# Kernel optimization log

Measured on AMD Instinct MI355X. Metric: run time of the kernel, lower is better.

## Reference

```python
import jax, jax.numpy as jnp
import numpy as np

N_TILES, NX = 6, 96
IN_C, HID_C = 128, 256
BATCH = 4


def _build_neighbors(n_tiles=N_TILES, nx=NX):
    # 4-connectivity on each tile with periodic wrap (fixed cubed-sphere-style
    # grid graph; preserves the gather/mean access pattern of build_dgl_graph).
    i, j = np.meshgrid(np.arange(nx), np.arange(nx), indexing='ij')
    idx = lambda ii, jj: (ii % nx) * nx + (jj % nx)
    per_tile = np.stack([idx(i - 1, j), idx(i + 1, j), idx(i, j - 1), idx(i, j + 1)],
                        axis=-1).reshape(nx * nx, 4)
    offsets = (np.arange(n_tiles) * nx * nx)[:, None, None]
    return (per_tile[None] + offsets).reshape(-1, 4).astype(np.int32)


def setup_inputs() -> dict:
    key = jax.random.key(0)
    ks = jax.random.split(key, 6)
    s = lambda fan_in: 1.0 / np.sqrt(fan_in)
    return {
        'x': jax.random.normal(ks[0], (BATCH, N_TILES, NX, NX, IN_C), jnp.float32),
        'neighbors': jnp.asarray(_build_neighbors()),
        'W_self1': jax.random.normal(ks[1], (IN_C, HID_C), jnp.float32) * s(IN_C),
        'W_neigh1': jax.random.normal(ks[2], (IN_C, HID_C), jnp.float32) * s(IN_C),
        'b1': jnp.zeros((HID_C,), jnp.float32),
        'W_self2': jax.random.normal(ks[3], (HID_C, HID_C), jnp.float32) * s(HID_C),
        'W_neigh2': jax.random.normal(ks[4], (HID_C, HID_C), jnp.float32) * s(HID_C),
        'b2': jnp.zeros((HID_C,), jnp.float32),
    }


def _sage_conv(h, neighbors, W_self, W_neigh, b):
    # h: [B, N, C]; neighbors: [N, 4] -> mean-aggregated SAGEConv
    h_neigh = jnp.mean(h[:, neighbors], axis=2)  # [B, N, 4, C] -> [B, N, C]
    return jnp.einsum('bnc,cd->bnd', h, W_self) + \
           jnp.einsum('bnc,cd->bnd', h_neigh, W_neigh) + b


def reference(x, neighbors, W_self1, W_neigh1, b1, W_self2, W_neigh2, b2):
    B, T, X, Y, C = x.shape
    h = x.reshape(B, T * X * Y, C)                      # flatten sphere -> nodes
    h = jax.nn.relu(_sage_conv(h, neighbors, W_self1, W_neigh1, b1))
    h = jax.nn.relu(_sage_conv(h, neighbors, W_self2, W_neigh2, b2))
    return h.reshape(B, T, X, Y, -1)
```

## Files before the change

kernel.cpp:

```cpp
#include <hip/hip_runtime.h>
#include <stdint.h>

typedef __attribute__((ext_vector_type(8))) short short8;
typedef __attribute__((ext_vector_type(4))) float f32x4;

#define NNODES 55296
#define DOUT 256

#define WAIT_VM(N) asm volatile("s_waitcnt vmcnt(" #N ")" ::: "memory")
#define SOFT_FENCE asm volatile("" ::: "memory")

__device__ __forceinline__ float bf2f(unsigned short h) {
    union { unsigned u; float f; } x; x.u = ((unsigned)h) << 16; return x.f;
}
__device__ __forceinline__ unsigned short f2bf(float f) {
    union { float f; unsigned u; } x; x.f = f;
    return (unsigned short)((x.u + 0x7fffu + ((x.u >> 16) & 1u)) >> 16);
}

__device__ __forceinline__ void storev(float* p, float v) { *p = v; }
__device__ __forceinline__ void storev(unsigned short* p, float v) { *p = f2bf(v); }

__device__ __forceinline__ void dma16(const void* g, void* l) {
    __builtin_amdgcn_global_load_lds(
        reinterpret_cast<const unsigned int __attribute__((address_space(1)))*>((uintptr_t)g),
        reinterpret_cast<unsigned int __attribute__((address_space(3)))*>((uintptr_t)l),
        16, 0, 0);
}

__device__ __forceinline__ short8 frag_self(const float* p) {
    float4 a = *(const float4*)p, b = *(const float4*)(p + 4);
    union { short8 s; unsigned short u[8]; } r;
    r.u[0] = f2bf(a.x); r.u[1] = f2bf(a.y); r.u[2] = f2bf(a.z); r.u[3] = f2bf(a.w);
    r.u[4] = f2bf(b.x); r.u[5] = f2bf(b.y); r.u[6] = f2bf(b.z); r.u[7] = f2bf(b.w);
    return r.s;
}
__device__ __forceinline__ short8 frag_self(const unsigned short* p) {
    return *(const short8*)p;
}
__device__ __forceinline__ void acc8(const float* p, float* o) {
    float4 a = *(const float4*)p, b = *(const float4*)(p + 4);
    o[0] += a.x; o[1] += a.y; o[2] += a.z; o[3] += a.w;
    o[4] += b.x; o[5] += b.y; o[6] += b.z; o[7] += b.w;
}
__device__ __forceinline__ void acc8(const unsigned short* p, float* o) {
    uint4 v = *(const uint4*)p;
    const unsigned short* u = (const unsigned short*)&v;
#pragma unroll
    for (int i = 0; i < 8; ++i) o[i] += bf2f(u[i]);
}
template <typename TIN>
__device__ __forceinline__ short8 frag_mean4(const TIN* p0, const TIN* p1,
                                             const TIN* p2, const TIN* p3) {
    float s[8] = {0.f, 0.f, 0.f, 0.f, 0.f, 0.f, 0.f, 0.f};
    acc8(p0, s); acc8(p1, s); acc8(p2, s); acc8(p3, s);
    union { short8 s8; unsigned short u[8]; } r;
#pragma unroll
    for (int i = 0; i < 8; ++i) r.u[i] = f2bf(s[i] * 0.25f);
    return r.s8;
}

__global__ void build_wt(const float* __restrict__ Ws,
                         const float* __restrict__ Wn,
                         unsigned short* __restrict__ Wt, int C) {
    int K2 = 2 * C;
    int idx = blockIdx.x * 256 + threadIdx.x;
    if (idx >= 256 * K2) return;
    int d = idx / K2;
    int k = idx - d * K2;
    float v = (k < C) ? Ws[(size_t)k * DOUT + d] : Wn[(size_t)(k - C) * DOUT + d];
    Wt[idx] = f2bf(v);
}

__global__ void build_wt_pm(const float* __restrict__ Ws,
                            const float* __restrict__ Wn,
                            unsigned short* __restrict__ Wp, int C) {
    int K2 = 2 * C;
    int idx = blockIdx.x * 256 + threadIdx.x;
    if (idx >= 256 * K2) return;
    int d = idx / K2;
    int k = idx - d * K2;
    float v = (k < C) ? Ws[(size_t)k * DOUT + d] : Wn[(size_t)(k - C) * DOUT + d];
    int q = k >> 6;
    int kqb = (k & 63) * 2;
    int byte = q * 32768 + d * 128 + (kqb ^ ((d & 7) << 4));
    Wp[byte >> 1] = f2bf(v);
}

__global__ __launch_bounds__(256) void mean_xb_pm(const float* __restrict__ x,
                                                  const int* __restrict__ nbr,
                                                  unsigned short* __restrict__ xm,
                                                  int mTot) {
    const int idx = blockIdx.x * 256 + threadIdx.x;
    const int node = idx >> 4;
    const int ch = (idx & 15) * 8;
    const int b = node / NNODES;
    const int n = node - b * NNODES;
    const size_t bbase = (size_t)b * NNODES;
    const int4 nb = *(const int4*)(nbr + (size_t)n * 4);
    const float* ps = x + (size_t)node * 128 + ch;
    union { uint4 v; unsigned short u[8]; } rs, rm;
    float4 a0 = *(const float4*)ps, a1 = *(const float4*)(ps + 4);
    rs.u[0] = f2bf(a0.x); rs.u[1] = f2bf(a0.y); rs.u[2] = f2bf(a0.z); rs.u[3] = f2bf(a0.w);
    rs.u[4] = f2bf(a1.x); rs.u[5] = f2bf(a1.y); rs.u[6] = f2bf(a1.z); rs.u[7] = f2bf(a1.w);
    float s[8] = {0.f, 0.f, 0.f, 0.f, 0.f, 0.f, 0.f, 0.f};
    acc8(x + (bbase + nb.x) * 128 + ch, s);
    acc8(x + (bbase + nb.y) * 128 + ch, s);
    acc8(x + (bbase + nb.z) * 128 + ch, s);
    acc8(x + (bbase + nb.w) * 128 + ch, s);
#pragma unroll
    for (int i = 0; i < 8; ++i) rm.u[i] = f2bf(s[i] * 0.25f);
    const size_t cs = (size_t)mTot * 32;
    *(uint4*)(xm + (size_t)(ch >> 5) * cs + (size_t)node * 32 + (ch & 31)) = rs.v;
    *(uint4*)(xm + (size_t)(4 + (ch >> 5)) * cs + (size_t)node * 32 + (ch & 31)) = rm.v;
}

__global__ __launch_bounds__(256) void mean_pass_pm(const unsigned short* __restrict__ h1,
                                                    const int* __restrict__ nbr,
                                                    unsigned short* __restrict__ hm,
                                                    int mTot) {
    const int idx = blockIdx.x * 256 + threadIdx.x;
    const int node = idx >> 5;
    const int ch = (idx & 31) * 8;
    const int b = node / NNODES;
    const int n = node - b * NNODES;
    const size_t bbase = (size_t)b * NNODES;
    const int4 nb = *(const int4*)(nbr + (size_t)n * 4);
    const size_t cs = (size_t)mTot * 32;
    const size_t co = (size_t)(ch >> 5) * cs + (ch & 31);
    float s[8] = {0.f, 0.f, 0.f, 0.f, 0.f, 0.f, 0.f, 0.f};
    acc8(h1 + co + (bbase + nb.x) * 32, s);
    acc8(h1 + co + (bbase + nb.y) * 32, s);
    acc8(h1 + co + (bbase + nb.z) * 32, s);
    acc8(h1 + co + (bbase + nb.w) * 32, s);
    union { uint4 v; unsigned short u[8]; } r;
#pragma unroll
    for (int i = 0; i < 8; ++i) r.u[i] = f2bf(s[i] * 0.25f);
    *(uint4*)(hm + co + (size_t)node * 32) = r.v;
}

template <int NK, typename TOUT>
__global__ __launch_bounds__(256) void sage_v15(
    const unsigned short* __restrict__ a0p,
    const unsigned short* __restrict__ a1p,
    const unsigned short* __restrict__ Wp,
    const float* __restrict__ bias,
    TOUT* __restrict__ out,
    int nwg, int mTot) {
    extern __shared__ char lds[];
    const int tid = threadIdx.x;
    const int bid = blockIdx.x;
    const int wk = (bid & 7) * (nwg >> 3) + (bid >> 3);
    const int yg = wk & 1;
    const int rb = wk >> 1;
    const int gcol0 = yg * 128;
    const int rowbase = rb * 128;

    const int l = tid & 63, w = tid >> 6;
    const int lr = l & 15, lg = l >> 4;
    const int rowg = w >> 1;
    const int colb = (w & 1) * 64;

    const size_t chstride = (size_t)mTot * 64;

    auto stageW = [&](int p) {
        char* wb = lds + ((p & 1) << 14);
        const char* src = (const char*)Wp + (size_t)p * 32768 + (size_t)gcol0 * 128;
#pragma unroll
        for (int i = 0; i < 4; ++i) {
            int o = w * 4096 + i * 1024;
            dma16(src + o + l * 16, wb + o + l * 16);
        }
    };
    auto issueA = [&](int p) {
        const char* base = (p >= 4) ? (const char*)a1p : (const char*)a0p;
        const char* src = base + (size_t)((2 * p) & 7) * chstride + (size_t)rowbase * 64;
        char* ring = lds + 32768 + (p % 3) * 16384;
#pragma unroll
        for (int s = 0; s < 2; ++s) {
            const char* cs_ = src + (size_t)s * chstride;
            char* dst = ring + s * 8192;
#pragma unroll
            for (int i = 0; i < 2; ++i) {
                int o = w * 2048 + i * 1024;
                dma16(cs_ + o + l * 16, dst + o + l * 16);
            }
        }
    };

    stageW(0); issueA(0); issueA(1);

    f32x4 acc[4][4];
#pragma unroll
    for (int m = 0; m < 4; ++m)
#pragma unroll
        for (int j = 0; j < 4; ++j) acc[m][j] = (f32x4){0.f, 0.f, 0.f, 0.f};

#pragma unroll
    for (int kk = 0; kk < NK; ++kk) {
        if (kk == NK - 1) { WAIT_VM(0); } else { WAIT_VM(4); }
        __builtin_amdgcn_s_barrier();
        SOFT_FENCE;

        if (kk + 1 < NK) stageW(kk + 1);
        if (kk + 2 < NK) issueA(kk + 2);

        const int ringo = 32768 + (kk % 3) * 16384;
        char* wbuf = lds + ((kk & 1) << 14);
#pragma unroll
        for (int sub = 0; sub < 2; ++sub) {
            short8 af[4];
#pragma unroll
            for (int m = 0; m < 4; ++m)
                af[m] = *(const short8*)(lds + ringo + sub * 8192 +
                                         ((rowg * 4 + m) * 16 + lr) * 64 + lg * 16);
            const int kq0 = (sub << 6) | (lg << 4);
#pragma unroll
            for (int j = 0; j < 4; ++j) {
                const int col = colb + j * 16 + lr;
                const short8 wf = *(const short8*)(
                    wbuf + (col << 7) + (kq0 ^ ((lr & 7) << 4)));
#pragma unroll
                for (int m = 0; m < 4; ++m)
                    acc[m][j] = __builtin_amdgcn_mfma_f32_16x16x32_bf16(wf, af[m], acc[m][j], 0, 0, 0);
            }
        }
        SOFT_FENCE;
    }

#pragma unroll
    for (int m = 0; m < 4; ++m) {
        const int row = rowbase + rowg * 64 + m * 16 + lr;
#pragma unroll
        for (int j = 0; j < 4; ++j) {
            const int gcol = gcol0 + colb + j * 16 + lg * 4;
            const float4 bv = *(const float4*)(bias + gcol);
            float o0 = fmaxf(acc[m][j][0] + bv.x, 0.f);
            float o1 = fmaxf(acc[m][j][1] + bv.y, 0.f);
            float o2 = fmaxf(acc[m][j][2] + bv.z, 0.f);
            float o3 = fmaxf(acc[m][j][3] + bv.w, 0.f);
            if constexpr (sizeof(TOUT) == 4) {
                float4 o = {o0, o1, o2, o3};
                *(float4*)((float*)out + (size_t)row * 256 + gcol) = o;
            } else {
                union { unsigned short u[4]; uint2 v; } pk;
                pk.u[0] = f2bf(o0); pk.u[1] = f2bf(o1);
                pk.u[2] = f2bf(o2); pk.u[3] = f2bf(o3);
                unsigned short* hp = (unsigned short*)out +
                    (size_t)(gcol >> 5) * ((size_t)mTot * 32) +
                    (size_t)row * 32 + (gcol & 31);
                *(uint2*)hp = pk.v;
            }
        }
    }
}

template <int C, typename TIN, typename TOUT>
__global__ __launch_bounds__(512, 2) void sage_v3(
    const TIN* __restrict__ hin, const int* __restrict__ nbr,
    const unsigned short* __restrict__ Wt, const float* __restrict__ bias,
    TOUT* __restrict__ out) {
    constexpr int K2 = 2 * C;
    constexpr int ROWB = K2 * 2;
    constexpr int LCOLS = 131072 / ROWB;
    constexpr int CG = LCOLS / 128;
    constexpr int RG = 8 / CG;
    extern __shared__ char Bs[];

    const int tid = threadIdx.x;
    const int gcol0 = blockIdx.y * LCOLS;
    {
        const char* src = (const char*)(Wt + (size_t)gcol0 * K2);
#pragma unroll
        for (int i = 0; i < 16; ++i) {
            int byt = (i * 512 + tid) * 16;
            uint4 v = *(const uint4*)(src + byt);
            int c = byt / ROWB;
            *(uint4*)(Bs + (byt ^ ((c & 7) << 4))) = v;
        }
    }
    __syncthreads();

    const int l = tid & 63;
    const int w = tid >> 6;
    const int rowg = w / CG;
    const int colb = (w % CG) * 128;
    const int lr = l & 15, lg = l >> 4;

    const int rowbase = blockIdx.x * (RG * 64) + rowg * 64;
    const int bb = rowbase / NNODES;
    const int n0 = rowbase - bb * NNODES;
    const size_t bbase = (size_t)bb * NNODES;

    unsigned soff[4], noff[4][4];
#pragma unroll
    for (int m = 0; m < 4; ++m) {
        int r = m * 16 + lr;
        soff[m] = (unsigned)(((rowbase + r) * (size_t)C + lg * 8) * sizeof(TIN));
        int4 nb = *(const int4*)(nbr + (size_t)(n0 + r) * 4);
        noff[m][0] = (unsigned)(((bbase + nb.x) * C + lg * 8) * sizeof(TIN));
        noff[m][1] = (unsigned)(((bbase + nb.y) * C + lg * 8) * sizeof(TIN));
        noff[m][2] = (unsigned)(((bbase + nb.z) * C + lg * 8) * sizeof(TIN));
        noff[m][3] = (unsigned)(((bbase + nb.w) * C + lg * 8) * sizeof(TIN));
    }
    const char* hb = (const char*)hin;

    f32x4 acc[4][8];
#pragma unroll
    for (int m = 0; m < 4; ++m)
#pragma unroll
        for (int j = 0; j < 8; ++j) acc[m][j] = (f32x4){0.f, 0.f, 0.f, 0.f};

#pragma unroll
    for (int kk = 0; kk < K2 / 32; ++kk) {
        const int k0 = kk * 32;
        short8 a[4];
        if (k0 < C) {
            const unsigned kb = k0 * sizeof(TIN);
#pragma unroll
            for (int m = 0; m < 4; ++m)
                a[m] = frag_self((const TIN*)(hb + soff[m] + kb));
        } else {
            const unsigned kb = (k0 - C) * sizeof(TIN);
#pragma unroll
            for (int m = 0; m < 4; ++m)
                a[m] = frag_mean4((const TIN*)(hb + noff[m][0] + kb),
                                  (const TIN*)(hb + noff[m][1] + kb),
                                  (const TIN*)(hb + noff[m][2] + kb),
                                  (const TIN*)(hb + noff[m][3] + kb));
        }
#pragma unroll
        for (int j = 0; j < 8; ++j) {
            const int c = colb + j * 16 + lr;
            const short8 bf = *(const short8*)(
                Bs + ((c * ROWB + (k0 + lg * 8) * 2) ^ ((l & 7) << 4)));
#pragma unroll
            for (int m = 0; m < 4; ++m)
                acc[m][j] = __builtin_amdgcn_mfma_f32_16x16x32_bf16(a[m], bf, acc[m][j], 0, 0, 0);
        }
    }

#pragma unroll
    for (int j = 0; j < 8; ++j) {
        const int gcol = gcol0 + colb + j * 16 + lr;
        const float bv = bias[gcol];
#pragma unroll
        for (int m = 0; m < 4; ++m) {
#pragma unroll
            for (int r = 0; r < 4; ++r) {
                const int row = rowbase + m * 16 + lg * 4 + r;
                storev(out + (size_t)row * DOUT + gcol, fmaxf(acc[m][j][r] + bv, 0.f));
            }
        }
    }
}

extern "C" void kernel_launch(void* const* d_in, const int* in_sizes, int n_in,
                              void* d_out, int out_size, void* d_ws, size_t ws_size,
                              hipStream_t stream) {
    const float* x = (const float*)d_in[0];
    const int* nbr = (const int*)d_in[1];
    const float* Ws1 = (const float*)d_in[2];
    const float* Wn1 = (const float*)d_in[3];
    const float* b1 = (const float*)d_in[4];
    const float* Ws2 = (const float*)d_in[5];
    const float* Wn2 = (const float*)d_in[6];
    const float* b2 = (const float*)d_in[7];
    float* out = (float*)d_out;

    const int B = in_sizes[0] / (NNODES * 128);
    const int M = B * NNODES;

    char* ws = (char*)d_ws;
    const size_t h1_bytes = (size_t)M * DOUT * 2;
    const size_t hm_bytes = (size_t)M * DOUT * 2;
    const size_t need = h1_bytes + hm_bytes + 131072 + 262144;

    if (ws_size >= need) {
        unsigned short* h1 = (unsigned short*)ws;
        unsigned short* xm = (unsigned short*)(ws + h1_bytes);
        unsigned short* W1p = (unsigned short*)(ws + h1_bytes + hm_bytes);
        unsigned short* W2p = W1p + 256 * 256;

        build_wt_pm<<<256, 256, 0, stream>>>(Ws1, Wn1, W1p, 128);
        build_wt_pm<<<512, 256, 0, stream>>>(Ws2, Wn2, W2p, 256);

        hipFuncSetAttribute((const void*)sage_v15<4, unsigned short>,
                            hipFuncAttributeMaxDynamicSharedMemorySize, 81920);
        hipFuncSetAttribute((const void*)sage_v15<8, float>,
                            hipFuncAttributeMaxDynamicSharedMemorySize, 81920);

        const int nwg = (M / 128) * 2;

        mean_xb_pm<<<M / 16, 256, 0, stream>>>(x, nbr, xm, M);
        sage_v15<4, unsigned short>
            <<<nwg, 256, 81920, stream>>>(xm, xm, W1p, b1, h1, nwg, M);
        mean_pass_pm<<<M / 8, 256, 0, stream>>>(h1, nbr, xm, M);
        sage_v15<8, float>
            <<<nwg, 256, 81920, stream>>>(h1, xm, W2p, b2, out, nwg, M);
    } else {
        unsigned short* h1 = (unsigned short*)ws;
        unsigned short* Wt1 = (unsigned short*)(ws + h1_bytes);
        unsigned short* Wt2 = Wt1 + 256 * 256;

        build_wt<<<256, 256, 0, stream>>>(Ws1, Wn1, Wt1, 128);
        build_wt<<<512, 256, 0, stream>>>(Ws2, Wn2, Wt2, 256);

        hipFuncSetAttribute((const void*)sage_v3<128, float, unsigned short>,
                            hipFuncAttributeMaxDynamicSharedMemorySize, 131072);
        hipFuncSetAttribute((const void*)sage_v3<256, unsigned short, float>,
                            hipFuncAttributeMaxDynamicSharedMemorySize, 131072);

        sage_v3<128, float, unsigned short>
            <<<dim3(M / 256, 1), 512, 131072, stream>>>(x, nbr, Wt1, b1, h1);
        sage_v3<256, unsigned short, float>
            <<<dim3(M / 512, 2), 512, 131072, stream>>>(h1, nbr, Wt2, b2, out);
    }
}
```

Measured before the change: 316.3 us.

## Load GEMM A operand directly into registers instead of LDS ring

Replaces the three-slot LDS ring for the activation operand with per-wave direct global loads into double-buffered registers, keeping only the weight tile in LDS. This cuts dynamic shared memory from 80KB to 32KB, which can allow more workgroups per CU and removes LDS reads for A. In exchange, waves sharing rows load A redundantly from global/L2, register pressure grows, and the full vmcnt(0) wait each step reduces overlap of prefetch with compute.

Result: slower. 355.3 us (+12.3%).

```diff
diff --git a/kernel.cpp b/kernel.cpp
--- a/kernel.cpp
+++ b/kernel.cpp
@@ -140,7 +140,7 @@
 }
 
 template <int NK, typename TOUT>
-__global__ __launch_bounds__(256) void sage_v15(
+__global__ __launch_bounds__(256) void sage_v16(
     const unsigned short* __restrict__ a0p,
     const unsigned short* __restrict__ a1p,
     const unsigned short* __restrict__ Wp,
@@ -172,23 +172,22 @@
             dma16(src + o + l * 16, wb + o + l * 16);
         }
     };
-    auto issueA = [&](int p) {
-        const char* base = (p >= 4) ? (const char*)a1p : (const char*)a0p;
-        const char* src = base + (size_t)((2 * p) & 7) * chstride + (size_t)rowbase * 64;
-        char* ring = lds + 32768 + (p % 3) * 16384;
-#pragma unroll
-        for (int s = 0; s < 2; ++s) {
-            const char* cs_ = src + (size_t)s * chstride;
-            char* dst = ring + s * 8192;
-#pragma unroll
-            for (int i = 0; i < 2; ++i) {
-                int o = w * 2048 + i * 1024;
-                dma16(cs_ + o + l * 16, dst + o + l * 16);
+    const unsigned aoff = (unsigned)(rowbase + rowg * 64 + lr) * 64 + (lg << 4);
+    auto loadA = [&](int p, short8 (&a)[4][2]) {
+        const char* base = (NK == 8 && p >= 4) ? (const char*)a1p : (const char*)a0p;
+#pragma unroll
+        for (int m = 0; m < 4; ++m)
+#pragma unroll
+            for (int sub = 0; sub < 2; ++sub) {
+                const int c = (2 * p + sub) & 7;
+                a[m][sub] = *(const short8*)(base + (size_t)c * chstride +
+                                             aoff + (unsigned)(m * 16) * 64);
             }
-        }
     };
 
-    stageW(0); issueA(0); issueA(1);
+    short8 aA[4][2], aB[4][2];
+    loadA(0, aA);
+    stageW(0);
 
     f32x4 acc[4][4];
 #pragma unroll
@@ -198,22 +197,19 @@
 
 #pragma unroll
     for (int kk = 0; kk < NK; ++kk) {
-        if (kk == NK - 1) { WAIT_VM(0); } else { WAIT_VM(4); }
+        WAIT_VM(0);
         __builtin_amdgcn_s_barrier();
         SOFT_FENCE;
 
-        if (kk + 1 < NK) stageW(kk + 1);
-        if (kk + 2 < NK) issueA(kk + 2);
-
-        const int ringo = 32768 + (kk % 3) * 16384;
+        if (kk + 1 < NK) {
+            if (kk & 1) loadA(kk + 1, aA); else loadA(kk + 1, aB);
+            stageW(kk + 1);
+        }
+
+        const short8(*cur)[2] = (kk & 1) ? aB : aA;
         char* wbuf = lds + ((kk & 1) << 14);
 #pragma unroll
         for (int sub = 0; sub < 2; ++sub) {
-            short8 af[4];
-#pragma unroll
-            for (int m = 0; m < 4; ++m)
-                af[m] = *(const short8*)(lds + ringo + sub * 8192 +
-                                         ((rowg * 4 + m) * 16 + lr) * 64 + lg * 16);
             const int kq0 = (sub << 6) | (lg << 4);
 #pragma unroll
             for (int j = 0; j < 4; ++j) {
@@ -222,7 +218,7 @@
                     wbuf + (col << 7) + (kq0 ^ ((lr & 7) << 4)));
 #pragma unroll
                 for (int m = 0; m < 4; ++m)
-                    acc[m][j] = __builtin_amdgcn_mfma_f32_16x16x32_bf16(wf, af[m], acc[m][j], 0, 0, 0);
+                    acc[m][j] = __builtin_amdgcn_mfma_f32_16x16x32_bf16(wf, cur[m][sub], acc[m][j], 0, 0, 0);
             }
         }
         SOFT_FENCE;
@@ -385,19 +381,19 @@
         build_wt_pm<<<256, 256, 0, stream>>>(Ws1, Wn1, W1p, 128);
         build_wt_pm<<<512, 256, 0, stream>>>(Ws2, Wn2, W2p, 256);
 
-        hipFuncSetAttribute((const void*)sage_v15<4, unsigned short>,
-                            hipFuncAttributeMaxDynamicSharedMemorySize, 81920);
-        hipFuncSetAttribute((const void*)sage_v15<8, float>,
-                            hipFuncAttributeMaxDynamicSharedMemorySize, 81920);
+        hipFuncSetAttribute((const void*)sage_v16<4, unsigned short>,
+                            hipFuncAttributeMaxDynamicSharedMemorySize, 32768);
+        hipFuncSetAttribute((const void*)sage_v16<8, float>,
+                            hipFuncAttributeMaxDynamicSharedMemorySize, 32768);
 
         const int nwg = (M / 128) * 2;
 
         mean_xb_pm<<<M / 16, 256, 0, stream>>>(x, nbr, xm, M);
-        sage_v15<4, unsigned short>
-            <<<nwg, 256, 81920, stream>>>(xm, xm, W1p, b1, h1, nwg, M);
+        sage_v16<4, unsigned short>
+            <<<nwg, 256, 32768, stream>>>(xm, xm, W1p, b1, h1, nwg, M);
         mean_pass_pm<<<M / 8, 256, 0, stream>>>(h1, nbr, xm, M);
-        sage_v15<8, float>
-            <<<nwg, 256, 81920, stream>>>(h1, xm, W2p, b2, out, nwg, M);
+        sage_v16<8, float>
+            <<<nwg, 256, 32768, stream>>>(h1, xm, W2p, b2, out, nwg, M);
     } else {
         unsigned short* h1 = (unsigned short*)ws;
         unsigned short* Wt1 = (unsigned short*)(ws + h1_bytes);
```
